# Kernel tuning notes

Hardware: AMD Instinct MI355X
Metric: run time of the kernel (lower is better)

The kernel has to match this reference:

```python
import jax, jax.numpy as jnp
import numpy as np

V0, V1, C = 64, 128, 128
V = V0 * V1  # product-graph node count = kron eigenvalue count


def setup_inputs() -> dict:
    key = jax.random.key(0)
    ks = jax.random.split(key, 8)
    x = jax.random.normal(ks[0], (V, C), dtype=jnp.float32)
    edge_index = jax.random.randint(ks[1], (2, 100), 0, V)  # unused on spectral path
    L = jnp.zeros((2, 2), dtype=jnp.float32)                # unused on spectral path
    mass = jax.random.uniform(ks[2], (V,), dtype=jnp.float32) + 0.5  # positive lumped mass
    evals0 = jax.random.uniform(ks[3], (V0,), dtype=jnp.float32) * 2.0  # factor-graph eigenvalues >= 0
    evals1 = jax.random.uniform(ks[4], (V1,), dtype=jnp.float32) * 2.0
    evecs = jax.random.normal(ks[5], (V, V), dtype=jnp.float32) / np.float32(np.sqrt(V))
    diffusion_time = jax.random.uniform(ks[6], (2, C), dtype=jnp.float32)  # nn.Parameter [P, C_inout]
    return {
        "x": x, "edge_index": edge_index, "L": L, "mass": mass,
        "evals0": evals0, "evals1": evals1, "evecs": evecs,
        "diffusion_time": diffusion_time,
    }


def reference(x, edge_index, L, mass, evals0, evals1, evecs, diffusion_time):
    # to_basis: project mass-weighted signal onto the spectral basis. [V,C]
    x_spec = evecs.T @ (x * mass[:, None])
    # Per-channel Kronecker diffusion coefficients:
    # kron(exp(-t0[c]*evals0), exp(-t1[c]*evals1)) for each channel c.
    e0 = jnp.exp(-evals0[:, None] * diffusion_time[0][None, :])  # [V0, C]
    e1 = jnp.exp(-evals1[:, None] * diffusion_time[1][None, :])  # [V1, C]
    diffusion_coefs = (e0[:, None, :] * e1[None, :, :]).reshape(V0 * V1, C)  # [V, C]
    # from_basis: back to node domain.
    x_diffuse = evecs @ (diffusion_coefs * x_spec)
    return x_diffuse
```

## Files before the change

### kernel.cpp

```cpp
#include <hip/hip_runtime.h>
#include <stdint.h>

#define V 8192
#define C 128
#define KS 4
#define KCH (V / KS)
#define BK 64
#define NI (KCH / BK)

typedef __attribute__((ext_vector_type(8))) short short8;
typedef __attribute__((ext_vector_type(4))) float floatx4;

static __device__ __forceinline__ unsigned short f2bf(float f) {
    unsigned u = __float_as_uint(f);
    u += 0x7FFF + ((u >> 16) & 1);
    return (unsigned short)(u >> 16);
}

static __device__ __forceinline__ void gload16(const void* g, void* l) {
    __builtin_amdgcn_global_load_lds(
        (const __attribute__((address_space(1))) void*)g,
        (__attribute__((address_space(3))) void*)l, 16, 0, 0);
}
#define SWAIT(s) asm volatile("s_waitcnt " s ::: "memory")
#define SBAR() __builtin_amdgcn_s_barrier()
#define SFENCE() __builtin_amdgcn_sched_barrier(0)

__global__ __launch_bounds__(256) void prep_xmt(const float* __restrict__ x,
                                                const float* __restrict__ mass,
                                                unsigned short* __restrict__ XMT) {
    __shared__ float tile[64][65];
    const int k0 = blockIdx.x * 64;
    const int c0 = blockIdx.y * 64;
    const int t = threadIdx.x;
#pragma unroll
    for (int p = 0; p < 16; ++p) {
        int idx = p * 256 + t;
        int kk = idx >> 6, cc = idx & 63;
        tile[kk][cc] = x[(size_t)(k0 + kk) * C + (c0 + cc)] * mass[k0 + kk];
    }
    __syncthreads();
#pragma unroll
    for (int p = 0; p < 16; ++p) {
        int idx = p * 256 + t;
        int cc = idx >> 6, kk = idx & 63;
        XMT[(size_t)(c0 + cc) * V + (k0 + kk)] = f2bf(tile[kk][cc]);
    }
}

__global__ __launch_bounds__(256, 2) void gemm1_p(const unsigned short* __restrict__ XMT,
                                                  const float* __restrict__ E,
                                                  float* __restrict__ P1) {
    __shared__ __align__(16) unsigned short ldsA[2][128 * BK];
    __shared__ __align__(16) unsigned short ldsB[2][64 * BK];
    const int bx = blockIdx.x;
    const int ks = bx >> 7;
    const int n0 = (bx & 127) * 64;
    const int kb = ks * KCH;
    const int t = threadIdx.x;
    const int w = t >> 6, lane = t & 63, q = lane >> 4, l15 = lane & 15;
    const int wm = (w & 1) * 64, wn = (w >> 1) * 32;
    const int lr = lane >> 3;
    const int lch = (lane & 7) ^ lr;
    const int jc = t & 15;
    const int vg = t >> 4;

    floatx4 acc[4][2] = {};
    float4 er0[4], er1[4];

#define G1_GLOADA(TI, BUF)                                                          \
    {                                                                               \
        const int kk_ = kb + (TI) * BK;                                             \
        _Pragma("unroll")                                                           \
        for (int i = 0; i < 4; ++i)                                                 \
            gload16(&XMT[(size_t)(i * 32 + w * 8 + lr) * V + kk_ + 8 * lch],        \
                    &ldsA[BUF][i * 2048 + w * 512]);                                \
    }
#define G1_ELOAD(ER, TI)                                                            \
    {                                                                               \
        const int kk_ = kb + (TI) * BK;                                             \
        _Pragma("unroll")                                                           \
        for (int u = 0; u < 4; ++u)                                                 \
            ER[u] = *(const float4*)&E[(size_t)(kk_ + vg * 4 + u) * V + n0 + jc * 4]; \
    }
#define G1_CONV(ER, BUF)                                                            \
    {                                                                               \
        _Pragma("unroll")                                                           \
        for (int jj = 0; jj < 4; ++jj) {                                            \
            const int j = jc * 4 + jj;                                              \
            ushort4 b;                                                              \
            b.x = f2bf(ER[0][jj]); b.y = f2bf(ER[1][jj]);                           \
            b.z = f2bf(ER[2][jj]); b.w = f2bf(ER[3][jj]);                           \
            *(ushort4*)&ldsB[BUF][j * BK + ((vg >> 1) ^ (j & 7)) * 8 + (vg & 1) * 4] = b; \
        }                                                                           \
    }
#define G1_MFMA(pA, pB)                                                             \
    {                                                                               \
        _Pragma("unroll")                                                           \
        for (int kk = 0; kk < BK; kk += 32) {                                       \
            short8 af[4], bfv[2];                                                   \
            _Pragma("unroll")                                                       \
            for (int mi = 0; mi < 4; ++mi) {                                        \
                const int m = wm + mi * 16 + l15;                                   \
                af[mi] = *(const short8*)&pA[m * BK + 8 * (((kk >> 3) + q) ^ (m & 7))]; \
            }                                                                       \
            _Pragma("unroll")                                                       \
            for (int ni = 0; ni < 2; ++ni) {                                        \
                const int n = wn + ni * 16 + l15;                                   \
                bfv[ni] = *(const short8*)&pB[n * BK + 8 * (((kk >> 3) + q) ^ (n & 7))]; \
            }                                                                       \
            _Pragma("unroll")                                                       \
            for (int mi = 0; mi < 4; ++mi)                                          \
                _Pragma("unroll")                                                   \
                for (int ni = 0; ni < 2; ++ni)                                      \
                    acc[mi][ni] = __builtin_amdgcn_mfma_f32_16x16x32_bf16(          \
                        af[mi], bfv[ni], acc[mi][ni], 0, 0, 0);                     \
        }                                                                           \
    }

    G1_ELOAD(er0, 0);
    G1_GLOADA(0, 0);
    G1_ELOAD(er1, 1);
    G1_CONV(er0, 0);
    SWAIT("vmcnt(4) lgkmcnt(0)");
    SBAR();
    SFENCE();

#define G1_BODY(T, PF_ER, CV_ER)                                                    \
    {                                                                               \
        const int t1 = (T) + 1;                                                     \
        const int t2 = ((T) + 2 < NI) ? (T) + 2 : NI - 1;                           \
        const bool pf = t1 < NI;                                                    \
        if (pf) {                                                                   \
            G1_GLOADA(t1, cur ^ 1);                                                 \
            G1_ELOAD(PF_ER, t2);                                                    \
        }                                                                           \
        SFENCE();                                                                   \
        __builtin_amdgcn_s_setprio(1);                                              \
        G1_MFMA((&ldsA[cur][0]), (&ldsB[cur][0]));                                  \
        __builtin_amdgcn_s_setprio(0);                                              \
        SFENCE();                                                                   \
        if (pf) {                                                                   \
            G1_CONV(CV_ER, cur ^ 1);                                                \
            SWAIT("vmcnt(4) lgkmcnt(0)");                                           \
            SBAR();                                                                 \
            SFENCE();                                                               \
            cur ^= 1;                                                               \
        }                                                                           \
    }

    int cur = 0;
    for (int tt = 0; tt < NI; tt += 2) {
        G1_BODY(tt, er0, er1);
        G1_BODY(tt + 1, er1, er0);
    }
#undef G1_BODY
#undef G1_MFMA
#undef G1_CONV
#undef G1_ELOAD
#undef G1_GLOADA

    float* Pks = P1 + (size_t)ks * C * V;
#pragma unroll
    for (int mi = 0; mi < 4; ++mi) {
        int mrow = wm + mi * 16 + q * 4;
#pragma unroll
        for (int ni = 0; ni < 2; ++ni) {
            int n = n0 + wn + ni * 16 + l15;
#pragma unroll
            for (int r = 0; r < 4; ++r)
                Pks[(size_t)(mrow + r) * V + n] = acc[mi][ni][r];
        }
    }
}

__global__ __launch_bounds__(256, 2) void gemm2_p(const float* __restrict__ E,
                                                  const unsigned short* __restrict__ YT,
                                                  float* __restrict__ P2) {
    __shared__ __align__(16) unsigned short ldsA[2][64 * BK];
    __shared__ __align__(16) unsigned short ldsB[2][128 * BK];
    const int bx = blockIdx.x;
    const int ks = bx >> 7;
    const int m0 = (bx & 127) * 64;
    const int kb = ks * KCH;
    const int t = threadIdx.x;
    const int w = t >> 6, lane = t & 63, q = lane >> 4, l15 = lane & 15;
    const int wm = (w & 1) * 32, wn = (w >> 1) * 64;
    const int lr = lane >> 3;
    const int lch = (lane & 7) ^ lr;
    const int ach = t & 15;
    const int arr = t >> 4;

    floatx4 acc[2][4] = {};
    float4 er0[4], er1[4];

#define G2_GLOADB(TI, BUF)                                                          \
    {                                                                               \
        const int kk_ = kb + (TI) * BK;                                             \
        _Pragma("unroll")                                                           \
        for (int i = 0; i < 4; ++i)                                                 \
            gload16(&YT[(size_t)(i * 32 + w * 8 + lr) * V + kk_ + 8 * lch],         \
                    &ldsB[BUF][i * 2048 + w * 512]);                                \
    }
#define G2_ELOAD(ER, TI)                                                            \
    {                                                                               \
        const int kk_ = kb + (TI) * BK;                                             \
        _Pragma("unroll")                                                           \
        for (int u = 0; u < 4; ++u)                                                 \
            ER[u] = *(const float4*)&E[(size_t)(m0 + arr + 16 * u) * V + kk_ + ach * 4]; \
    }
#define G2_CONV(ER, BUF)                                                            \
    {                                                                               \
        _Pragma("unroll")                                                           \
        for (int u = 0; u < 4; ++u) {                                               \
            const int row = arr + 16 * u;                                           \
            ushort4 av;                                                             \
            av.x = f2bf(ER[u].x); av.y = f2bf(ER[u].y);                             \
            av.z = f2bf(ER[u].z); av.w = f2bf(ER[u].w);                             \
            *(ushort4*)&ldsA[BUF][row * BK + ((ach >> 1) ^ (row & 7)) * 8 + (ach & 1) * 4] = av; \
        }                                                                           \
    }
#define G2_MFMA(pA, pB)                                                             \
    {                                                                               \
        _Pragma("unroll")                                                           \
        for (int kk = 0; kk < BK; kk += 32) {                                       \
            short8 af[2], bfv[4];                                                   \
            _Pragma("unroll")                                                       \
            for (int mi = 0; mi < 2; ++mi) {                                        \
                const int m = wm + mi * 16 + l15;                                   \
                af[mi] = *(const short8*)&pA[m * BK + 8 * (((kk >> 3) + q) ^ (m & 7))]; \
            }                                                                       \
            _Pragma("unroll")                                                       \
            for (int ni = 0; ni < 4; ++ni) {                                        \
                const int n = wn + ni * 16 + l15;                                   \
                bfv[ni] = *(const short8*)&pB[n * BK + 8 * (((kk >> 3) + q) ^ (n & 7))]; \
            }                                                                       \
            _Pragma("unroll")                                                       \
            for (int mi = 0; mi < 2; ++mi)                                          \
                _Pragma("unroll")                                                   \
                for (int ni = 0; ni < 4; ++ni)                                      \
                    acc[mi][ni] = __builtin_amdgcn_mfma_f32_16x16x32_bf16(          \
                        af[mi], bfv[ni], acc[mi][ni], 0, 0, 0);                     \
        }                                                                           \
    }

    G2_ELOAD(er0, 0);
    G2_GLOADB(0, 0);
    G2_ELOAD(er1, 1);
    G2_CONV(er0, 0);
    SWAIT("vmcnt(4) lgkmcnt(0)");
    SBAR();
    SFENCE();

#define G2_BODY(T, PF_ER, CV_ER)                                                    \
    {                                                                               \
        const int t1 = (T) + 1;                                                     \
        const int t2 = ((T) + 2 < NI) ? (T) + 2 : NI - 1;                           \
        const bool pf = t1 < NI;                                                    \
        if (pf) {                                                                   \
            G2_GLOADB(t1, cur ^ 1);                                                 \
            G2_ELOAD(PF_ER, t2);                                                    \
        }                                                                           \
        SFENCE();                                                                   \
        __builtin_amdgcn_s_setprio(1);                                              \
        G2_MFMA((&ldsA[cur][0]), (&ldsB[cur][0]));                                  \
        __builtin_amdgcn_s_setprio(0);                                              \
        SFENCE();                                                                   \
        if (pf) {                                                                   \
            G2_CONV(CV_ER, cur ^ 1);                                                \
            SWAIT("vmcnt(4) lgkmcnt(0)");                                           \
            SBAR();                                                                 \
            SFENCE();                                                               \
            cur ^= 1;                                                               \
        }                                                                           \
    }

    int cur = 0;
    for (int tt = 0; tt < NI; tt += 2) {
        G2_BODY(tt, er0, er1);
        G2_BODY(tt + 1, er1, er0);
    }
#undef G2_BODY
#undef G2_MFMA
#undef G2_CONV
#undef G2_ELOAD
#undef G2_GLOADB

    float* Pks = P2 + (size_t)ks * V * C;
#pragma unroll
    for (int mi = 0; mi < 2; ++mi) {
        int mrow = m0 + wm + mi * 16 + q * 4;
#pragma unroll
        for (int ni = 0; ni < 4; ++ni) {
            int n = wn + ni * 16 + l15;
#pragma unroll
            for (int r = 0; r < 4; ++r)
                Pks[(size_t)(mrow + r) * C + n] = acc[mi][ni][r];
        }
    }
}

__global__ __launch_bounds__(256) void red1(const float* __restrict__ P1,
                                            const float* __restrict__ ev0,
                                            const float* __restrict__ ev1,
                                            const float* __restrict__ dt,
                                            unsigned short* __restrict__ YT) {
    int id = blockIdx.x * 256 + threadIdx.x;
    int c = id >> 10;
    int j0 = (id & 1023) * 8;
    float s[8] = {};
#pragma unroll
    for (int ks = 0; ks < KS; ++ks) {
        const float* row = &P1[((size_t)ks * C + c) * V + j0];
        float4 a = *(const float4*)row;
        float4 b = *(const float4*)(row + 4);
        s[0] += a.x; s[1] += a.y; s[2] += a.z; s[3] += a.w;
        s[4] += b.x; s[5] += b.y; s[6] += b.z; s[7] += b.w;
    }
    float t0 = dt[c], t1 = dt[C + c];
    float a0 = ev0[j0 >> 7] * t0;
    short8 yv;
#pragma unroll
    for (int jj = 0; jj < 8; ++jj) {
        float coef = __expf(-(a0 + ev1[(j0 + jj) & 127] * t1));
        yv[jj] = (short)f2bf(s[jj] * coef);
    }
    *(short8*)&YT[(size_t)c * V + j0] = yv;
}

__global__ __launch_bounds__(256) void red2(const float* __restrict__ P2,
                                            float* __restrict__ out) {
    int id = blockIdx.x * 256 + threadIdx.x;
    size_t off = (size_t)id * 4;
    float4 s = {0.f, 0.f, 0.f, 0.f};
#pragma unroll
    for (int ks = 0; ks < KS; ++ks) {
        float4 v = *(const float4*)&P2[(size_t)ks * V * C + off];
        s.x += v.x; s.y += v.y; s.z += v.z; s.w += v.w;
    }
    *(float4*)&out[off] = s;
}

extern "C" void kernel_launch(void* const* d_in, const int* in_sizes, int n_in,
                              void* d_out, int out_size, void* d_ws, size_t ws_size,
                              hipStream_t stream) {
    const float* x    = (const float*)d_in[0];
    const float* mass = (const float*)d_in[3];
    const float* ev0  = (const float*)d_in[4];
    const float* ev1  = (const float*)d_in[5];
    const float* E    = (const float*)d_in[6];
    const float* dt   = (const float*)d_in[7];
    float* out = (float*)d_out;

    unsigned short* XMT = (unsigned short*)d_ws;
    unsigned short* YT  = XMT + (size_t)V * C;
    float* P = (float*)(YT + (size_t)V * C);

    prep_xmt<<<dim3(V / 64, C / 64), 256, 0, stream>>>(x, mass, XMT);
    gemm1_p<<<(V / 64) * KS, 256, 0, stream>>>(XMT, E, P);
    red1<<<(C * V / 8) / 256, 256, 0, stream>>>(P, ev0, ev1, dt, YT);
    gemm2_p<<<(V / 64) * KS, 256, 0, stream>>>(E, YT, P);
    red2<<<(V * C / 4) / 256, 256, 0, stream>>>(P, out);
}
```

Baseline: 443.3 us.

## Fuse five kernels into one persistent kernel with atomic-counter grid sync

Replaces the prep, two GEMM and two reduction launches with a single persistent kernel of 512 blocks. Phases are ordered with global atomic counters and spin-waits, and the counters are grouped per column so the second GEMM can start on a k-split as soon as its matching YT chunk is ready. The final reduction is done by whichever block is last to finish each slab. This removes launch gaps and tail idling between stages. In exchange it depends on all 512 blocks being resident at once (256 threads, two per CU), adds a memset and fence/atomic overhead, and the spin-wait has a guard that can silently break out.

```diff
diff --git a/kernel.cpp b/kernel.cpp
--- a/kernel.cpp
+++ b/kernel.cpp
@@ -7,6 +7,7 @@
 #define KCH (V / KS)
 #define BK 64
 #define NI (KCH / BK)
+#define NBLK 512
 
 typedef __attribute__((ext_vector_type(8))) short short8;
 typedef __attribute__((ext_vector_type(4))) float floatx4;
@@ -26,47 +27,82 @@
 #define SBAR() __builtin_amdgcn_s_barrier()
 #define SFENCE() __builtin_amdgcn_sched_barrier(0)
 
-__global__ __launch_bounds__(256) void prep_xmt(const float* __restrict__ x,
-                                                const float* __restrict__ mass,
-                                                unsigned short* __restrict__ XMT) {
-    __shared__ float tile[64][65];
-    const int k0 = blockIdx.x * 64;
-    const int c0 = blockIdx.y * 64;
-    const int t = threadIdx.x;
-#pragma unroll
-    for (int p = 0; p < 16; ++p) {
-        int idx = p * 256 + t;
-        int kk = idx >> 6, cc = idx & 63;
-        tile[kk][cc] = x[(size_t)(k0 + kk) * C + (c0 + cc)] * mass[k0 + kk];
-    }
+static __device__ __forceinline__ void block_signal(int* p) {
+    __threadfence();
     __syncthreads();
-#pragma unroll
-    for (int p = 0; p < 16; ++p) {
-        int idx = p * 256 + t;
-        int cc = idx >> 6, kk = idx & 63;
-        XMT[(size_t)(c0 + cc) * V + (k0 + kk)] = f2bf(tile[kk][cc]);
-    }
-}
-
-__global__ __launch_bounds__(256, 2) void gemm1_p(const unsigned short* __restrict__ XMT,
+    if (threadIdx.x == 0)
+        __hip_atomic_fetch_add(p, 1, __ATOMIC_RELEASE, __HIP_MEMORY_SCOPE_AGENT);
+}
+static __device__ __forceinline__ void block_wait(int* p, int target) {
+    if (threadIdx.x == 0) {
+        int guard = 0;
+        while (__hip_atomic_load(p, __ATOMIC_ACQUIRE, __HIP_MEMORY_SCOPE_AGENT) < target) {
+            __builtin_amdgcn_s_sleep(2);
+            if (++guard > (1 << 24)) break;
+        }
+    }
+    __syncthreads();
+    __threadfence();
+}
+
+__global__ __launch_bounds__(256, 2) void persist(const float* __restrict__ x,
+                                                  const float* __restrict__ mass,
                                                   const float* __restrict__ E,
-                                                  float* __restrict__ P1) {
-    __shared__ __align__(16) unsigned short ldsA[2][128 * BK];
-    __shared__ __align__(16) unsigned short ldsB[2][64 * BK];
-    const int bx = blockIdx.x;
-    const int ks = bx >> 7;
-    const int n0 = (bx & 127) * 64;
-    const int kb = ks * KCH;
+                                                  const float* __restrict__ ev0,
+                                                  const float* __restrict__ ev1,
+                                                  const float* __restrict__ dt,
+                                                  unsigned short* __restrict__ XMT,
+                                                  unsigned short* __restrict__ YT,
+                                                  float* __restrict__ P1,
+                                                  float* __restrict__ P2,
+                                                  float* __restrict__ out,
+                                                  int* __restrict__ cnt) {
+    __shared__ __align__(16) unsigned short LBIG[2][128 * BK];
+    __shared__ __align__(16) unsigned short LSML[2][64 * BK];
+    __shared__ int s_old;
+
+    const int bid = blockIdx.x;
     const int t = threadIdx.x;
     const int w = t >> 6, lane = t & 63, q = lane >> 4, l15 = lane & 15;
-    const int wm = (w & 1) * 64, wn = (w >> 1) * 32;
-    const int lr = lane >> 3;
-    const int lch = (lane & 7) ^ lr;
-    const int jc = t & 15;
-    const int vg = t >> 4;
-
-    floatx4 acc[4][2] = {};
-    float4 er0[4], er1[4];
+    const int lr = lane >> 3, lch = (lane & 7) ^ lr;
+    const int ks = bid >> 7;
+    const int slab = bid & 127;
+    const int kb = ks * KCH;
+
+    int* cnt_prep = cnt;
+    int* cnt_col = cnt + 16;
+    int* cnt_yt = cnt + 32;
+    int* cnt_m = cnt + 64;
+
+    if (bid < 256) {
+        float* tile = (float*)&LBIG[0][0];
+        const int k0 = (bid >> 1) * 64;
+        const int c0 = (bid & 1) * 64;
+#pragma unroll
+        for (int p = 0; p < 16; ++p) {
+            int idx = p * 256 + t;
+            int kk = idx >> 6, cc = idx & 63;
+            tile[kk * 65 + cc] = x[(size_t)(k0 + kk) * C + (c0 + cc)] * mass[k0 + kk];
+        }
+        __syncthreads();
+#pragma unroll
+        for (int p = 0; p < 16; ++p) {
+            int idx = p * 256 + t;
+            int cc = idx >> 6, kk = idx & 63;
+            XMT[(size_t)(c0 + cc) * V + (k0 + kk)] = f2bf(tile[kk * 65 + cc]);
+        }
+        block_signal(cnt_prep);
+    }
+    block_wait(cnt_prep, 256);
+
+    {
+        const int n0 = slab * 64;
+        const int wm = (w & 1) * 64, wn = (w >> 1) * 32;
+        const int jc = t & 15;
+        const int vg = t >> 4;
+
+        floatx4 acc[4][2] = {};
+        float4 er0[4], er1[4];
 
 #define G1_GLOADA(TI, BUF)                                                          \
     {                                                                               \
@@ -74,7 +110,7 @@
         _Pragma("unroll")                                                           \
         for (int i = 0; i < 4; ++i)                                                 \
             gload16(&XMT[(size_t)(i * 32 + w * 8 + lr) * V + kk_ + 8 * lch],        \
-                    &ldsA[BUF][i * 2048 + w * 512]);                                \
+                    &LBIG[BUF][i * 2048 + w * 512]);                                \
     }
 #define G1_ELOAD(ER, TI)                                                            \
     {                                                                               \
@@ -91,7 +127,7 @@
             ushort4 b;                                                              \
             b.x = f2bf(ER[0][jj]); b.y = f2bf(ER[1][jj]);                           \
             b.z = f2bf(ER[2][jj]); b.w = f2bf(ER[3][jj]);                           \
-            *(ushort4*)&ldsB[BUF][j * BK + ((vg >> 1) ^ (j & 7)) * 8 + (vg & 1) * 4] = b; \
+            *(ushort4*)&LSML[BUF][j * BK + ((vg >> 1) ^ (j & 7)) * 8 + (vg & 1) * 4] = b; \
         }                                                                           \
     }
 #define G1_MFMA(pA, pB)                                                             \
@@ -118,13 +154,13 @@
         }                                                                           \
     }
 
-    G1_ELOAD(er0, 0);
-    G1_GLOADA(0, 0);
-    G1_ELOAD(er1, 1);
-    G1_CONV(er0, 0);
-    SWAIT("vmcnt(4) lgkmcnt(0)");
-    SBAR();
-    SFENCE();
+        G1_ELOAD(er0, 0);
+        G1_GLOADA(0, 0);
+        G1_ELOAD(er1, 1);
+        G1_CONV(er0, 0);
+        SWAIT("vmcnt(4) lgkmcnt(0)");
+        SBAR();
+        SFENCE();
 
 #define G1_BODY(T, PF_ER, CV_ER)                                                    \
     {                                                                               \
@@ -137,7 +173,7 @@
         }                                                                           \
         SFENCE();                                                                   \
         __builtin_amdgcn_s_setprio(1);                                              \
-        G1_MFMA((&ldsA[cur][0]), (&ldsB[cur][0]));                                  \
+        G1_MFMA((&LBIG[cur][0]), (&LSML[cur][0]));                                  \
         __builtin_amdgcn_s_setprio(0);                                              \
         SFENCE();                                                                   \
         if (pf) {                                                                   \
@@ -149,50 +185,71 @@
         }                                                                           \
     }
 
-    int cur = 0;
-    for (int tt = 0; tt < NI; tt += 2) {
-        G1_BODY(tt, er0, er1);
-        G1_BODY(tt + 1, er1, er0);
-    }
+        int cur = 0;
+        for (int tt = 0; tt < NI; tt += 2) {
+            G1_BODY(tt, er0, er1);
+            G1_BODY(tt + 1, er1, er0);
+        }
 #undef G1_BODY
 #undef G1_MFMA
 #undef G1_CONV
 #undef G1_ELOAD
 #undef G1_GLOADA
 
-    float* Pks = P1 + (size_t)ks * C * V;
-#pragma unroll
-    for (int mi = 0; mi < 4; ++mi) {
-        int mrow = wm + mi * 16 + q * 4;
-#pragma unroll
-        for (int ni = 0; ni < 2; ++ni) {
-            int n = n0 + wn + ni * 16 + l15;
-#pragma unroll
-            for (int r = 0; r < 4; ++r)
-                Pks[(size_t)(mrow + r) * V + n] = acc[mi][ni][r];
-        }
-    }
-}
-
-__global__ __launch_bounds__(256, 2) void gemm2_p(const float* __restrict__ E,
-                                                  const unsigned short* __restrict__ YT,
-                                                  float* __restrict__ P2) {
-    __shared__ __align__(16) unsigned short ldsA[2][64 * BK];
-    __shared__ __align__(16) unsigned short ldsB[2][128 * BK];
-    const int bx = blockIdx.x;
-    const int ks = bx >> 7;
-    const int m0 = (bx & 127) * 64;
-    const int kb = ks * KCH;
-    const int t = threadIdx.x;
-    const int w = t >> 6, lane = t & 63, q = lane >> 4, l15 = lane & 15;
-    const int wm = (w & 1) * 32, wn = (w >> 1) * 64;
-    const int lr = lane >> 3;
-    const int lch = (lane & 7) ^ lr;
-    const int ach = t & 15;
-    const int arr = t >> 4;
-
-    floatx4 acc[2][4] = {};
-    float4 er0[4], er1[4];
+        float* Pks = P1 + (size_t)ks * C * V;
+#pragma unroll
+        for (int mi = 0; mi < 4; ++mi) {
+            int mrow = wm + mi * 16 + q * 4;
+#pragma unroll
+            for (int ni = 0; ni < 2; ++ni) {
+                int n = n0 + wn + ni * 16 + l15;
+#pragma unroll
+                for (int r = 0; r < 4; ++r)
+                    Pks[(size_t)(mrow + r) * V + n] = acc[mi][ni][r];
+            }
+        }
+    }
+    block_signal(cnt_col + (slab >> 5));
+
+    if (ks == 0) {
+        block_wait(cnt_col + (slab >> 5), 128);
+        const int j0s = slab * 64;
+#pragma unroll
+        for (int p = 0; p < 4; ++p) {
+            const int u = t + 256 * p;
+            const int c = u >> 3;
+            const int j0 = j0s + (u & 7) * 8;
+            float s[8] = {};
+#pragma unroll
+            for (int kr = 0; kr < KS; ++kr) {
+                const float* row = &P1[((size_t)kr * C + c) * V + j0];
+                float4 a = *(const float4*)row;
+                float4 b = *(const float4*)(row + 4);
+                s[0] += a.x; s[1] += a.y; s[2] += a.z; s[3] += a.w;
+                s[4] += b.x; s[5] += b.y; s[6] += b.z; s[7] += b.w;
+            }
+            const float t0 = dt[c], t1 = dt[C + c];
+            const float a0 = ev0[j0 >> 7] * t0;
+            short8 yv;
+#pragma unroll
+            for (int jj = 0; jj < 8; ++jj) {
+                float coef = __expf(-(a0 + ev1[(j0 + jj) & 127] * t1));
+                yv[jj] = (short)f2bf(s[jj] * coef);
+            }
+            *(short8*)&YT[(size_t)c * V + j0] = yv;
+        }
+        block_signal(cnt_yt + (slab >> 5));
+    }
+
+    block_wait(cnt_yt + ks, 32);
+    {
+        const int m0 = slab * 64;
+        const int wm = (w & 1) * 32, wn = (w >> 1) * 64;
+        const int ach = t & 15;
+        const int arr = t >> 4;
+
+        floatx4 acc[2][4] = {};
+        float4 er0[4], er1[4];
 
 #define G2_GLOADB(TI, BUF)                                                          \
     {                                                                               \
@@ -200,7 +257,7 @@
         _Pragma("unroll")                                                           \
         for (int i = 0; i < 4; ++i)                                                 \
             gload16(&YT[(size_t)(i * 32 + w * 8 + lr) * V + kk_ + 8 * lch],         \
-                    &ldsB[BUF][i * 2048 + w * 512]);                                \
+                    &LBIG[BUF][i * 2048 + w * 512]);                                \
     }
 #define G2_ELOAD(ER, TI)                                                            \
     {                                                                               \
@@ -217,7 +274,7 @@
             ushort4 av;                                                             \
             av.x = f2bf(ER[u].x); av.y = f2bf(ER[u].y);                             \
             av.z = f2bf(ER[u].z); av.w = f2bf(ER[u].w);                             \
-            *(ushort4*)&ldsA[BUF][row * BK + ((ach >> 1) ^ (row & 7)) * 8 + (ach & 1) * 4] = av; \
+            *(ushort4*)&LSML[BUF][row * BK + ((ach >> 1) ^ (row & 7)) * 8 + (ach & 1) * 4] = av; \
         }                                                                           \
     }
 #define G2_MFMA(pA, pB)                                                             \
@@ -244,13 +301,13 @@
         }                                                                           \
     }
 
-    G2_ELOAD(er0, 0);
-    G2_GLOADB(0, 0);
-    G2_ELOAD(er1, 1);
-    G2_CONV(er0, 0);
-    SWAIT("vmcnt(4) lgkmcnt(0)");
-    SBAR();
-    SFENCE();
+        G2_ELOAD(er0, 0);
+        G2_GLOADB(0, 0);
+        G2_ELOAD(er1, 1);
+        G2_CONV(er0, 0);
+        SWAIT("vmcnt(4) lgkmcnt(0)");
+        SBAR();
+        SFENCE();
 
 #define G2_BODY(T, PF_ER, CV_ER)                                                    \
     {                                                                               \
@@ -263,7 +320,7 @@
         }                                                                           \
         SFENCE();                                                                   \
         __builtin_amdgcn_s_setprio(1);                                              \
-        G2_MFMA((&ldsA[cur][0]), (&ldsB[cur][0]));                                  \
+        G2_MFMA((&LSML[cur][0]), (&LBIG[cur][0]));                                  \
         __builtin_amdgcn_s_setprio(0);                                              \
         SFENCE();                                                                   \
         if (pf) {                                                                   \
@@ -275,70 +332,53 @@
         }                                                                           \
     }
 
-    int cur = 0;
-    for (int tt = 0; tt < NI; tt += 2) {
-        G2_BODY(tt, er0, er1);
-        G2_BODY(tt + 1, er1, er0);
-    }
+        int cur = 0;
+        for (int tt = 0; tt < NI; tt += 2) {
+            G2_BODY(tt, er0, er1);
+            G2_BODY(tt + 1, er1, er0);
+        }
 #undef G2_BODY
 #undef G2_MFMA
 #undef G2_CONV
 #undef G2_ELOAD
 #undef G2_GLOADB
 
-    float* Pks = P2 + (size_t)ks * V * C;
-#pragma unroll
-    for (int mi = 0; mi < 2; ++mi) {
-        int mrow = m0 + wm + mi * 16 + q * 4;
-#pragma unroll
-        for (int ni = 0; ni < 4; ++ni) {
-            int n = wn + ni * 16 + l15;
-#pragma unroll
-            for (int r = 0; r < 4; ++r)
-                Pks[(size_t)(mrow + r) * C + n] = acc[mi][ni][r];
-        }
-    }
-}
-
-__global__ __launch_bounds__(256) void red1(const float* __restrict__ P1,
-                                            const float* __restrict__ ev0,
-                                            const float* __restrict__ ev1,
-                                            const float* __restrict__ dt,
-                                            unsigned short* __restrict__ YT) {
-    int id = blockIdx.x * 256 + threadIdx.x;
-    int c = id >> 10;
-    int j0 = (id & 1023) * 8;
-    float s[8] = {};
-#pragma unroll
-    for (int ks = 0; ks < KS; ++ks) {
-        const float* row = &P1[((size_t)ks * C + c) * V + j0];
-        float4 a = *(const float4*)row;
-        float4 b = *(const float4*)(row + 4);
-        s[0] += a.x; s[1] += a.y; s[2] += a.z; s[3] += a.w;
-        s[4] += b.x; s[5] += b.y; s[6] += b.z; s[7] += b.w;
-    }
-    float t0 = dt[c], t1 = dt[C + c];
-    float a0 = ev0[j0 >> 7] * t0;
-    short8 yv;
-#pragma unroll
-    for (int jj = 0; jj < 8; ++jj) {
-        float coef = __expf(-(a0 + ev1[(j0 + jj) & 127] * t1));
-        yv[jj] = (short)f2bf(s[jj] * coef);
-    }
-    *(short8*)&YT[(size_t)c * V + j0] = yv;
-}
-
-__global__ __launch_bounds__(256) void red2(const float* __restrict__ P2,
-                                            float* __restrict__ out) {
-    int id = blockIdx.x * 256 + threadIdx.x;
-    size_t off = (size_t)id * 4;
-    float4 s = {0.f, 0.f, 0.f, 0.f};
-#pragma unroll
-    for (int ks = 0; ks < KS; ++ks) {
-        float4 v = *(const float4*)&P2[(size_t)ks * V * C + off];
-        s.x += v.x; s.y += v.y; s.z += v.z; s.w += v.w;
-    }
-    *(float4*)&out[off] = s;
+        float* Pks = P2 + (size_t)ks * V * C;
+#pragma unroll
+        for (int mi = 0; mi < 2; ++mi) {
+            int mrow = m0 + wm + mi * 16 + q * 4;
+#pragma unroll
+            for (int ni = 0; ni < 4; ++ni) {
+                int n = wn + ni * 16 + l15;
+#pragma unroll
+                for (int r = 0; r < 4; ++r)
+                    Pks[(size_t)(mrow + r) * C + n] = acc[mi][ni][r];
+            }
+        }
+    }
+
+    __threadfence();
+    __syncthreads();
+    if (t == 0)
+        s_old = __hip_atomic_fetch_add(cnt_m + slab, 1, __ATOMIC_ACQ_REL,
+                                       __HIP_MEMORY_SCOPE_AGENT);
+    __syncthreads();
+    if (s_old == KS - 1) {
+        __threadfence();
+        const int m0 = slab * 64;
+#pragma unroll
+        for (int p = 0; p < 8; ++p) {
+            const int u = t + 256 * p;
+            const size_t off = (size_t)(m0 + (u >> 5)) * C + (u & 31) * 4;
+            float4 s = {0.f, 0.f, 0.f, 0.f};
+#pragma unroll
+            for (int kr = 0; kr < KS; ++kr) {
+                float4 v = *(const float4*)&P2[(size_t)kr * V * C + off];
+                s.x += v.x; s.y += v.y; s.z += v.z; s.w += v.w;
+            }
+            *(float4*)&out[off] = s;
+        }
+    }
 }
 
 extern "C" void kernel_launch(void* const* d_in, const int* in_sizes, int n_in,
@@ -352,13 +392,13 @@
     const float* dt   = (const float*)d_in[7];
     float* out = (float*)d_out;
 
-    unsigned short* XMT = (unsigned short*)d_ws;
+    int* cnt = (int*)d_ws;
+    unsigned short* XMT = (unsigned short*)((char*)d_ws + 16384);
     unsigned short* YT  = XMT + (size_t)V * C;
-    float* P = (float*)(YT + (size_t)V * C);
-
-    prep_xmt<<<dim3(V / 64, C / 64), 256, 0, stream>>>(x, mass, XMT);
-    gemm1_p<<<(V / 64) * KS, 256, 0, stream>>>(XMT, E, P);
-    red1<<<(C * V / 8) / 256, 256, 0, stream>>>(P, ev0, ev1, dt, YT);
-    gemm2_p<<<(V / 64) * KS, 256, 0, stream>>>(E, YT, P);
-    red2<<<(V * C / 4) / 256, 256, 0, stream>>>(P, out);
-}
+    float* P1 = (float*)(YT + (size_t)V * C);
+    float* P2 = P1 + (size_t)KS * C * V;
+
+    hipMemsetAsync(d_ws, 0, 16384, stream);
+    persist<<<NBLK, 256, 0, stream>>>(x, mass, E, ev0, ev1, dt, XMT, YT, P1, P2,
+                                      out, cnt);
+}
```

Result: slower. 879.4 us (+98.4%).
